# Performance work log

Hardware: AMD Instinct MI355X
Metric: run time of the kernel (lower is better)

## Reference

```python
import jax, jax.numpy as jnp
import numpy as np


def setup_inputs() -> dict:
    key = jax.random.key(0)
    ks = jax.random.split(key, 10)
    T, B, I, H, Z = 1024, 512, 128, 256, 1
    s = 0.1  # small init scale for stable recurrence
    return {
        "inputs": jax.random.normal(ks[0], (T, B, I), dtype=jnp.float32),
        "h0": jax.random.normal(ks[1], (B, H), dtype=jnp.float32) * s,
        "c0": jax.random.normal(ks[2], (B, H), dtype=jnp.float32) * s,
        "z0": jax.random.normal(ks[3], (B, Z), dtype=jnp.float32) * s,
        "W_ih": jax.random.normal(ks[4], (4 * H, I + Z), dtype=jnp.float32) * s,
        "W_hh": jax.random.normal(ks[5], (4 * H, H), dtype=jnp.float32) * s,
        "b_ih": jax.random.normal(ks[6], (4 * H,), dtype=jnp.float32) * s,
        "b_hh": jax.random.normal(ks[7], (4 * H,), dtype=jnp.float32) * s,
        "W_fc": jax.random.normal(ks[8], (Z, H), dtype=jnp.float32) * s,
        "b_fc": jax.random.normal(ks[9], (Z,), dtype=jnp.float32) * s,
    }


def reference(inputs, h0, c0, z0, W_ih, W_hh, b_ih, b_hh, W_fc, b_fc):
    def step(carry, x_t):
        h, c, z = carry
        xz = jnp.concatenate([x_t, z], axis=1)  # [B, I+Z]
        gates = xz @ W_ih.T + b_ih + h @ W_hh.T + b_hh  # [B, 4H]
        i_g, f_g, g_g, o_g = jnp.split(gates, 4, axis=1)  # torch gate order i,f,g,o
        i_g = jax.nn.sigmoid(i_g)
        f_g = jax.nn.sigmoid(f_g)
        g_g = jnp.tanh(g_g)
        o_g = jax.nn.sigmoid(o_g)
        c = f_g * c + i_g * g_g
        h = o_g * jnp.tanh(c)
        z = jnp.tanh(h @ W_fc.T + b_fc)  # [B, Z]
        return (h, c, z), z

    (h, c, _), outputs = jax.lax.scan(step, (h0, c0, z0), inputs)
    return outputs, h, c  # outputs: [T, B, Z]
```

## Files before the change

### kernel.cpp

```cpp
#include <hip/hip_runtime.h>
#include <hip/hip_bf16.h>
#include <stdint.h>

#define TT 1024
#define BB 512
#define II 128
#define HH 256
#define NKC 12
#define GSTR 132

typedef __attribute__((ext_vector_type(8))) short bf16x8;
typedef __attribute__((ext_vector_type(4))) float f32x4;
typedef __attribute__((ext_vector_type(4))) uint32_t u32x4;
typedef unsigned long long ull;

__device__ __forceinline__ float fsig(float x)  { return 1.0f / (1.0f + __expf(-x)); }
__device__ __forceinline__ float ftanh(float x) { return 1.0f - 2.0f / (__expf(2.0f * x) + 1.0f); }
__device__ __forceinline__ uint16_t f2bf(float f) {
    return __bfloat16_as_ushort(__float2bfloat16(f));
}
__device__ __forceinline__ float bf2lo(uint32_t w) { return __uint_as_float(w << 16); }
__device__ __forceinline__ float bf2hi(uint32_t w) { return __uint_as_float(w & 0xffff0000u); }

template<int DUAL>
__global__ __launch_bounds__(512, 1) void lstm_kernel(
    const float* __restrict__ x,
    const float* __restrict__ h0, const float* __restrict__ c0,
    const float* __restrict__ z0,
    const float* __restrict__ W_ih, const float* __restrict__ W_hh,
    const float* __restrict__ b_ih, const float* __restrict__ b_hh,
    const float* __restrict__ Wfc, const float* __restrict__ bfc,
    ull* __restrict__ hbF, ull* __restrict__ hbS,
    float* __restrict__ out)
{
    __shared__ __align__(16) uint16_t a_sh[NKC * 4 * 16 * 8];
    __shared__ float g_sh[16 * GSTR];
    __shared__ float zp_sh[2][8][16];

    const int tid  = threadIdx.x;
    const int lane = tid & 63, wv = tid >> 6;
    const int bid  = blockIdx.x;
    const int mm   = bid >> 3;
    const int role = mm & 7, grp = (bid & 7) * 4 + (mm >> 3);
    const int b0   = grp * 16;
    const int arow = tid >> 5, auu = tid & 31;
    const int u_g  = role * 32 + auu;
    const int xc   = (tid & 31) * 4;
    const int grole = wv, grow = (tid >> 2) & 15, gwq = tid & 3;

    bf16x8 wreg[NKC];
    {
        int lc = wv * 16 + (lane & 15);
        int col = (lc >> 5) * 256 + role * 32 + (lc & 31);
        #pragma unroll
        for (int kc = 0; kc < NKC; ++kc) {
            int k0 = kc * 32 + (lane >> 4) * 8;
            const float* src = (k0 < II) ? &W_ih[(size_t)col * (II + 1) + k0]
                                         : &W_hh[(size_t)col * HH + (k0 - II)];
            bf16x8 wv8;
            #pragma unroll
            for (int j = 0; j < 8; ++j) wv8[j] = (short)f2bf(src[j]);
            wreg[kc] = wv8;
        }
    }

    float bia[4], wzv[4];
    #pragma unroll
    for (int g = 0; g < 4; ++g) {
        int c = g * 256 + u_g;
        bia[g] = b_ih[c] + b_hh[c];
        wzv[g] = W_ih[(size_t)c * (II + 1) + II];
    }
    float wfc8[8];
    #pragma unroll
    for (int j = 0; j < 8; ++j) wfc8[j] = Wfc[grole * 32 + gwq * 8 + j];
    const float wfc  = Wfc[u_g];
    const float bfcs = bfc[0];
    const float z0r  = z0[b0 + arow];
    float c_r = c0[(size_t)(b0 + arow) * HH + u_g];

    {
        const float* hp = h0 + (size_t)(b0 + grow) * HH + grole * 32 + gwq * 8;
        uint4 pw;
        pw.x = (uint32_t)f2bf(hp[0]) | ((uint32_t)f2bf(hp[1]) << 16);
        pw.y = (uint32_t)f2bf(hp[2]) | ((uint32_t)f2bf(hp[3]) << 16);
        pw.z = (uint32_t)f2bf(hp[4]) | ((uint32_t)f2bf(hp[5]) << 16);
        pw.w = (uint32_t)f2bf(hp[6]) | ((uint32_t)f2bf(hp[7]) << 16);
        *(uint4*)&a_sh[(((4 + grole) * 4 + gwq) * 16 + grow) * 8] = pw;
    }
    {
        float4 xv = *(const float4*)&x[(size_t)(b0 + arow) * II + xc];
        int kcx = xc >> 5, gx = (xc >> 3) & 3, jx = xc & 7;
        ushort4 p;
        p.x = f2bf(xv.x); p.y = f2bf(xv.y); p.z = f2bf(xv.z); p.w = f2bf(xv.w);
        *(ushort4*)&a_sh[((kcx * 4 + gx) * 16 + arow) * 8 + jx] = p;
    }

    for (int t = 0; t <= TT; ++t) {
        float4 xn = make_float4(0.f, 0.f, 0.f, 0.f);
        if (t + 1 < TT)
            xn = *(const float4*)&x[(size_t)(t + 1) * (BB * II) + (size_t)(b0 + arow) * II + xc];

        if (t > 0 && grole != role) {
            const int par = (t - 1) & 1;
            const size_t gidx = ((((size_t)par * 32 + grp) * 8 + grole) * 16 + grow) * 16
                              + gwq * 4;
            const ull* pF = hbF + gidx;
            const ull* pS = hbS + gidx;
            u32x4 a0, a1;
            uint32_t it = 0;
            const uint32_t tt = (uint32_t)t;
            for (;;) {
                if (DUAL) {
                    u32x4 f0, f1;
                    asm volatile(
                        "global_load_dwordx4 %0, %2, off sc0\n\t"
                        "global_load_dwordx4 %1, %2, off offset:16 sc0\n\t"
                        "s_waitcnt vmcnt(0)"
                        : "=&v"(f0), "=&v"(f1) : "v"(pF) : "memory");
                    if (min(min(f0.y, f0.w), min(f1.y, f1.w)) >= tt) { a0 = f0; a1 = f1; break; }
                    ++it;
                    if ((it & 7) != 0) { __builtin_amdgcn_s_sleep(1); continue; }
                }
                u32x4 s0, s1;
                asm volatile(
                    "global_load_dwordx4 %0, %2, off sc0 sc1\n\t"
                    "global_load_dwordx4 %1, %2, off offset:16 sc0 sc1\n\t"
                    "s_waitcnt vmcnt(0)"
                    : "=&v"(s0), "=&v"(s1) : "v"(pS) : "memory");
                if (min(min(s0.y, s0.w), min(s1.y, s1.w)) >= tt) { a0 = s0; a1 = s1; break; }
                __builtin_amdgcn_s_sleep(1);
                if (!DUAL) ++it;
                if (it > (1u << 20)) { a0 = s0; a1 = s1; break; }
            }
            uint32_t w0 = a0.x, w1 = a0.z, w2 = a1.x, w3 = a1.z;
            uint4 pw; pw.x = w0; pw.y = w1; pw.z = w2; pw.w = w3;
            *(uint4*)&a_sh[(((4 + grole) * 4 + gwq) * 16 + grow) * 8] = pw;
            float p = bf2lo(w0) * wfc8[0] + bf2hi(w0) * wfc8[1]
                    + bf2lo(w1) * wfc8[2] + bf2hi(w1) * wfc8[3]
                    + bf2lo(w2) * wfc8[4] + bf2hi(w2) * wfc8[5]
                    + bf2lo(w3) * wfc8[6] + bf2hi(w3) * wfc8[7];
            p += __shfl_xor(p, 1, 64);
            p += __shfl_xor(p, 2, 64);
            if (gwq == 0) zp_sh[t & 1][grole][grow] = p;
        }
        __syncthreads();

        if (t == TT) {
            if (role == 0 && tid < 16) {
                float s = bfcs;
                #pragma unroll
                for (int r = 0; r < 8; ++r) s += zp_sh[TT & 1][r][tid];
                out[(size_t)(TT - 1) * BB + b0 + tid] = ftanh(s);
            }
            break;
        }

        f32x4 acc0 = {0.f, 0.f, 0.f, 0.f}, acc1 = {0.f, 0.f, 0.f, 0.f};
        #pragma unroll
        for (int kc = 0; kc < NKC; kc += 2) {
            bf16x8 a0 = *(const bf16x8*)&a_sh[((kc * 4 + (lane >> 4)) * 16 + (lane & 15)) * 8];
            acc0 = __builtin_amdgcn_mfma_f32_16x16x32_bf16(a0, wreg[kc], acc0, 0, 0, 0);
            bf16x8 a1 = *(const bf16x8*)&a_sh[(((kc + 1) * 4 + (lane >> 4)) * 16 + (lane & 15)) * 8];
            acc1 = __builtin_amdgcn_mfma_f32_16x16x32_bf16(a1, wreg[kc + 1], acc1, 0, 0, 0);
        }
        f32x4 acc = acc0 + acc1;
        {
            int r0 = (lane >> 4) * 4, cb = wv * 16 + (lane & 15);
            #pragma unroll
            for (int i = 0; i < 4; ++i) g_sh[(r0 + i) * GSTR + cb] = acc[i];
        }
        __syncthreads();

        {
            int kcx = xc >> 5, gx = (xc >> 3) & 3, jx = xc & 7;
            ushort4 p;
            p.x = f2bf(xn.x); p.y = f2bf(xn.y); p.z = f2bf(xn.z); p.w = f2bf(xn.w);
            *(ushort4*)&a_sh[((kcx * 4 + gx) * 16 + arow) * 8 + jx] = p;
        }

        float zp_;
        if (t == 0) {
            zp_ = z0r;
        } else {
            float s = bfcs;
            #pragma unroll
            for (int r = 0; r < 8; ++r) s += zp_sh[t & 1][r][arow];
            zp_ = ftanh(s);
            if (role == 0 && auu == 0)
                out[(size_t)(t - 1) * BB + b0 + arow] = zp_;
        }
        float gi = g_sh[arow * GSTR +      auu] + bia[0] + wzv[0] * zp_;
        float gf = g_sh[arow * GSTR + 32 + auu] + bia[1] + wzv[1] * zp_;
        float gg = g_sh[arow * GSTR + 64 + auu] + bia[2] + wzv[2] * zp_;
        float go = g_sh[arow * GSTR + 96 + auu] + bia[3] + wzv[3] * zp_;
        float ig = fsig(gi), fg = fsig(gf), gc = ftanh(gg), og = fsig(go);
        float cn = fg * c_r + ig * gc;
        c_r = cn;
        float hn = og * ftanh(cn);

        uint32_t hb16 = f2bf(hn);
        uint32_t nb = __shfl_down(hb16, 1, 64);
        if (!(auu & 1)) {
            uint32_t word = hb16 | (nb << 16);
            *(uint32_t*)&a_sh[(((4 + role) * 4 + (auu >> 3)) * 16 + arow) * 8 + (auu & 7)]
                = word;
            ull q = ((ull)(uint32_t)(t + 1) << 32) | (ull)word;
            size_t o = ((((size_t)(t & 1) * 32 + grp) * 8 + role) * 16 + arow) * 16
                     + (auu >> 1);
            if (DUAL)
                asm volatile("global_store_dwordx2 %0, %1, off sc0"
                             :: "v"(hbF + o), "v"(q) : "memory");
            asm volatile("global_store_dwordx2 %0, %1, off sc0 sc1"
                         :: "v"(hbS + o), "v"(q) : "memory");
        }
        float pz = hn * wfc;
        #pragma unroll
        for (int off = 16; off >= 1; off >>= 1) pz += __shfl_xor(pz, off, 32);
        if (auu == 0) zp_sh[(t + 1) & 1][role][arow] = pz;

        if (t == TT - 1) {
            size_t ho = (size_t)TT * BB + (size_t)(b0 + arow) * HH + u_g;
            out[ho] = hn;
            out[ho + (size_t)BB * HH] = cn;
        }
    }
}

extern "C" void kernel_launch(void* const* d_in, const int* in_sizes, int n_in,
                              void* d_out, int out_size, void* d_ws, size_t ws_size,
                              hipStream_t stream) {
    const float* x    = (const float*)d_in[0];
    const float* h0   = (const float*)d_in[1];
    const float* c0   = (const float*)d_in[2];
    const float* z0   = (const float*)d_in[3];
    const float* W_ih = (const float*)d_in[4];
    const float* W_hh = (const float*)d_in[5];
    const float* b_ih = (const float*)d_in[6];
    const float* b_hh = (const float*)d_in[7];
    const float* Wfc  = (const float*)d_in[8];
    const float* bfc  = (const float*)d_in[9];
    float* out = (float*)d_out;

    const size_t COPY = (size_t)2 * 32 * 8 * 16 * 16 * 8;
    if (ws_size >= 2 * COPY) {
        ull* hbF = (ull*)d_ws;
        ull* hbS = (ull*)((char*)d_ws + COPY);
        hipMemsetAsync(d_ws, 0, 2 * COPY, stream);
        lstm_kernel<1><<<256, 512, 0, stream>>>(x, h0, c0, z0, W_ih, W_hh,
                                                b_ih, b_hh, Wfc, bfc,
                                                hbF, hbS, out);
    } else {
        ull* hbS = (ull*)d_ws;
        hipMemsetAsync(d_ws, 0, COPY, stream);
        lstm_kernel<0><<<256, 512, 0, stream>>>(x, h0, c0, z0, W_ih, W_hh,
                                                b_ih, b_hh, Wfc, bfc,
                                                hbS, hbS, out);
    }
}
```

Before: 2.185 ms.

## Remove a barrier per step, restage x loads, and cap spin-wait fallback

Moves the x conversion and LDS store to the top of the next step, with loads issued early by only four waves, so the second __syncthreads between the MFMA and the x write is gone. The h exchange lane mapping changes so each wave's z partial reduces with cross-half shuffles, and the fast-path poll now checks the slow coherent copy every fourth iteration instead of every eighth. An adaptive cap ('strikes') shortens the spin timeout once timeouts recur, which may let a block proceed with stale data. The DUAL template is dropped, so the single-buffer fallback still issues both stores to the same buffer.

Result: slower. 2.512 ms (+14.9%).

```diff
diff --git a/kernel.cpp b/kernel.cpp
--- a/kernel.cpp
+++ b/kernel.cpp
@@ -22,7 +22,6 @@
 __device__ __forceinline__ float bf2lo(uint32_t w) { return __uint_as_float(w << 16); }
 __device__ __forceinline__ float bf2hi(uint32_t w) { return __uint_as_float(w & 0xffff0000u); }
 
-template<int DUAL>
 __global__ __launch_bounds__(512, 1) void lstm_kernel(
     const float* __restrict__ x,
     const float* __restrict__ h0, const float* __restrict__ c0,
@@ -45,8 +44,8 @@
     const int b0   = grp * 16;
     const int arow = tid >> 5, auu = tid & 31;
     const int u_g  = role * 32 + auu;
-    const int xc   = (tid & 31) * 4;
-    const int grole = wv, grow = (tid >> 2) & 15, gwq = tid & 3;
+    const int grole = wv, grow = lane & 15, gwq = lane >> 4;
+    const int xrow = lane & 15, xoct = lane >> 4;
 
     bf16x8 wreg[NKC];
     {
@@ -88,18 +87,33 @@
         pw.w = (uint32_t)f2bf(hp[6]) | ((uint32_t)f2bf(hp[7]) << 16);
         *(uint4*)&a_sh[(((4 + grole) * 4 + gwq) * 16 + grow) * 8] = pw;
     }
-    {
-        float4 xv = *(const float4*)&x[(size_t)(b0 + arow) * II + xc];
-        int kcx = xc >> 5, gx = (xc >> 3) & 3, jx = xc & 7;
-        ushort4 p;
-        p.x = f2bf(xv.x); p.y = f2bf(xv.y); p.z = f2bf(xv.z); p.w = f2bf(xv.w);
-        *(ushort4*)&a_sh[((kcx * 4 + gx) * 16 + arow) * 8 + jx] = p;
-    }
-
+    float4 xA = make_float4(0.f, 0.f, 0.f, 0.f), xB = xA;
+    if (wv < 4) {
+        const float* xs = &x[(size_t)(b0 + xrow) * II + wv * 32 + xoct * 8];
+        float4 u0 = *(const float4*)xs, u1 = *(const float4*)(xs + 4);
+        ushort4 lo, hi;
+        lo.x = f2bf(u0.x); lo.y = f2bf(u0.y); lo.z = f2bf(u0.z); lo.w = f2bf(u0.w);
+        hi.x = f2bf(u1.x); hi.y = f2bf(u1.y); hi.z = f2bf(u1.z); hi.w = f2bf(u1.w);
+        int de = ((wv * 4 + xoct) * 16 + xrow) * 8;
+        *(ushort4*)&a_sh[de] = lo;
+        *(ushort4*)&a_sh[de + 4] = hi;
+        if (TT > 1) {
+            const float* xs1 = &x[(size_t)(BB * II) + (size_t)(b0 + xrow) * II + wv * 32 + xoct * 8];
+            xA = *(const float4*)xs1;
+            xB = *(const float4*)(xs1 + 4);
+        }
+    }
+
+    uint32_t strikes = 0;
     for (int t = 0; t <= TT; ++t) {
-        float4 xn = make_float4(0.f, 0.f, 0.f, 0.f);
-        if (t + 1 < TT)
-            xn = *(const float4*)&x[(size_t)(t + 1) * (BB * II) + (size_t)(b0 + arow) * II + xc];
+        if (wv < 4 && t > 0 && t < TT) {
+            ushort4 lo, hi;
+            lo.x = f2bf(xA.x); lo.y = f2bf(xA.y); lo.z = f2bf(xA.z); lo.w = f2bf(xA.w);
+            hi.x = f2bf(xB.x); hi.y = f2bf(xB.y); hi.z = f2bf(xB.z); hi.w = f2bf(xB.w);
+            int de = ((wv * 4 + xoct) * 16 + xrow) * 8;
+            *(ushort4*)&a_sh[de] = lo;
+            *(ushort4*)&a_sh[de + 4] = hi;
+        }
 
         if (t > 0 && grole != role) {
             const int par = (t - 1) & 1;
@@ -109,19 +123,18 @@
             const ull* pS = hbS + gidx;
             u32x4 a0, a1;
             uint32_t it = 0;
+            const uint32_t cap = (strikes >= 4) ? 64u : (1u << 18);
             const uint32_t tt = (uint32_t)t;
             for (;;) {
-                if (DUAL) {
-                    u32x4 f0, f1;
-                    asm volatile(
-                        "global_load_dwordx4 %0, %2, off sc0\n\t"
-                        "global_load_dwordx4 %1, %2, off offset:16 sc0\n\t"
-                        "s_waitcnt vmcnt(0)"
-                        : "=&v"(f0), "=&v"(f1) : "v"(pF) : "memory");
-                    if (min(min(f0.y, f0.w), min(f1.y, f1.w)) >= tt) { a0 = f0; a1 = f1; break; }
-                    ++it;
-                    if ((it & 7) != 0) { __builtin_amdgcn_s_sleep(1); continue; }
-                }
+                u32x4 f0, f1;
+                asm volatile(
+                    "global_load_dwordx4 %0, %2, off sc0\n\t"
+                    "global_load_dwordx4 %1, %2, off offset:16 sc0\n\t"
+                    "s_waitcnt vmcnt(0)"
+                    : "=&v"(f0), "=&v"(f1) : "v"(pF) : "memory");
+                if (min(min(f0.y, f0.w), min(f1.y, f1.w)) >= tt) { a0 = f0; a1 = f1; break; }
+                ++it;
+                if ((it & 3) != 0) { __builtin_amdgcn_s_sleep(1); continue; }
                 u32x4 s0, s1;
                 asm volatile(
                     "global_load_dwordx4 %0, %2, off sc0 sc1\n\t"
@@ -130,8 +143,7 @@
                     : "=&v"(s0), "=&v"(s1) : "v"(pS) : "memory");
                 if (min(min(s0.y, s0.w), min(s1.y, s1.w)) >= tt) { a0 = s0; a1 = s1; break; }
                 __builtin_amdgcn_s_sleep(1);
-                if (!DUAL) ++it;
-                if (it > (1u << 20)) { a0 = s0; a1 = s1; break; }
+                if (it > cap) { ++strikes; a0 = s0; a1 = s1; break; }
             }
             uint32_t w0 = a0.x, w1 = a0.z, w2 = a1.x, w3 = a1.z;
             uint4 pw; pw.x = w0; pw.y = w1; pw.z = w2; pw.w = w3;
@@ -140,9 +152,16 @@
                     + bf2lo(w1) * wfc8[2] + bf2hi(w1) * wfc8[3]
                     + bf2lo(w2) * wfc8[4] + bf2hi(w2) * wfc8[5]
                     + bf2lo(w3) * wfc8[6] + bf2hi(w3) * wfc8[7];
-            p += __shfl_xor(p, 1, 64);
-            p += __shfl_xor(p, 2, 64);
+            p += __shfl_xor(p, 16, 64);
+            p += __shfl_xor(p, 32, 64);
             if (gwq == 0) zp_sh[t & 1][grole][grow] = p;
+        }
+
+        if (wv < 4 && t + 1 < TT) {
+            const float* xs1 = &x[(size_t)(t + 1) * (BB * II)
+                                  + (size_t)(b0 + xrow) * II + wv * 32 + xoct * 8];
+            xA = *(const float4*)xs1;
+            xB = *(const float4*)(xs1 + 4);
         }
         __syncthreads();
 
@@ -154,29 +173,6 @@
                 out[(size_t)(TT - 1) * BB + b0 + tid] = ftanh(s);
             }
             break;
-        }
-
-        f32x4 acc0 = {0.f, 0.f, 0.f, 0.f}, acc1 = {0.f, 0.f, 0.f, 0.f};
-        #pragma unroll
-        for (int kc = 0; kc < NKC; kc += 2) {
-            bf16x8 a0 = *(const bf16x8*)&a_sh[((kc * 4 + (lane >> 4)) * 16 + (lane & 15)) * 8];
-            acc0 = __builtin_amdgcn_mfma_f32_16x16x32_bf16(a0, wreg[kc], acc0, 0, 0, 0);
-            bf16x8 a1 = *(const bf16x8*)&a_sh[(((kc + 1) * 4 + (lane >> 4)) * 16 + (lane & 15)) * 8];
-            acc1 = __builtin_amdgcn_mfma_f32_16x16x32_bf16(a1, wreg[kc + 1], acc1, 0, 0, 0);
-        }
-        f32x4 acc = acc0 + acc1;
-        {
-            int r0 = (lane >> 4) * 4, cb = wv * 16 + (lane & 15);
-            #pragma unroll
-            for (int i = 0; i < 4; ++i) g_sh[(r0 + i) * GSTR + cb] = acc[i];
-        }
-        __syncthreads();
-
-        {
-            int kcx = xc >> 5, gx = (xc >> 3) & 3, jx = xc & 7;
-            ushort4 p;
-            p.x = f2bf(xn.x); p.y = f2bf(xn.y); p.z = f2bf(xn.z); p.w = f2bf(xn.w);
-            *(ushort4*)&a_sh[((kcx * 4 + gx) * 16 + arow) * 8 + jx] = p;
         }
 
         float zp_;
@@ -190,6 +186,23 @@
             if (role == 0 && auu == 0)
                 out[(size_t)(t - 1) * BB + b0 + arow] = zp_;
         }
+
+        f32x4 acc0 = {0.f, 0.f, 0.f, 0.f}, acc1 = {0.f, 0.f, 0.f, 0.f};
+        #pragma unroll
+        for (int kc = 0; kc < NKC; kc += 2) {
+            bf16x8 a0 = *(const bf16x8*)&a_sh[((kc * 4 + (lane >> 4)) * 16 + (lane & 15)) * 8];
+            acc0 = __builtin_amdgcn_mfma_f32_16x16x32_bf16(a0, wreg[kc], acc0, 0, 0, 0);
+            bf16x8 a1 = *(const bf16x8*)&a_sh[(((kc + 1) * 4 + (lane >> 4)) * 16 + (lane & 15)) * 8];
+            acc1 = __builtin_amdgcn_mfma_f32_16x16x32_bf16(a1, wreg[kc + 1], acc1, 0, 0, 0);
+        }
+        f32x4 acc = acc0 + acc1;
+        {
+            int r0 = (lane >> 4) * 4, cb = wv * 16 + (lane & 15);
+            #pragma unroll
+            for (int i = 0; i < 4; ++i) g_sh[(r0 + i) * GSTR + cb] = acc[i];
+        }
+        __syncthreads();
+
         float gi = g_sh[arow * GSTR +      auu] + bia[0] + wzv[0] * zp_;
         float gf = g_sh[arow * GSTR + 32 + auu] + bia[1] + wzv[1] * zp_;
         float gg = g_sh[arow * GSTR + 64 + auu] + bia[2] + wzv[2] * zp_;
@@ -208,9 +221,8 @@
             ull q = ((ull)(uint32_t)(t + 1) << 32) | (ull)word;
             size_t o = ((((size_t)(t & 1) * 32 + grp) * 8 + role) * 16 + arow) * 16
                      + (auu >> 1);
-            if (DUAL)
-                asm volatile("global_store_dwordx2 %0, %1, off sc0"
-                             :: "v"(hbF + o), "v"(q) : "memory");
+            asm volatile("global_store_dwordx2 %0, %1, off sc0"
+                         :: "v"(hbF + o), "v"(q) : "memory");
             asm volatile("global_store_dwordx2 %0, %1, off sc0 sc1"
                          :: "v"(hbS + o), "v"(q) : "memory");
         }
@@ -247,14 +259,12 @@
         ull* hbF = (ull*)d_ws;
         ull* hbS = (ull*)((char*)d_ws + COPY);
         hipMemsetAsync(d_ws, 0, 2 * COPY, stream);
-        lstm_kernel<1><<<256, 512, 0, stream>>>(x, h0, c0, z0, W_ih, W_hh,
-                                                b_ih, b_hh, Wfc, bfc,
-                                                hbF, hbS, out);
+        lstm_kernel<<<256, 512, 0, stream>>>(x, h0, c0, z0, W_ih, W_hh, b_ih, b_hh,
+                                             Wfc, bfc, hbF, hbS, out);
     } else {
-        ull* hbS = (ull*)d_ws;
+        ull* hb = (ull*)d_ws;
         hipMemsetAsync(d_ws, 0, COPY, stream);
-        lstm_kernel<0><<<256, 512, 0, stream>>>(x, h0, c0, z0, W_ih, W_hh,
-                                                b_ih, b_hh, Wfc, bfc,
-                                                hbS, hbS, out);
+        lstm_kernel<<<256, 512, 0, stream>>>(x, h0, c0, z0, W_ih, W_hh, b_ih, b_hh,
+                                             Wfc, bfc, hb, hb, out);
     }
 }
```

## Rework inter-block spin-wait polling, lane mapping, and single-buffer zp reduction

Applied to the files above, without the earlier changes.

Drops the DUAL template and always polls the fast (sc0) flag buffer, falling back to the system-coherent copy every fourth iteration instead of every eighth. It adds a strike counter that caps spinning at a small iteration count once timeouts have occurred. The gather lane mapping changes so the z partial reduction uses xor-16/32 shuffles, and the zp shared buffer drops double-buffering. The intent is lower cross-block handoff latency per step. The risk is that the timeout cap could consume stale h data, and the single-buffered zp_sh may race across steps.

Result: no change. 2.211 ms (+1.2%).

```diff
diff --git a/kernel.cpp b/kernel.cpp
--- a/kernel.cpp
+++ b/kernel.cpp
@@ -22,7 +22,6 @@
 __device__ __forceinline__ float bf2lo(uint32_t w) { return __uint_as_float(w << 16); }
 __device__ __forceinline__ float bf2hi(uint32_t w) { return __uint_as_float(w & 0xffff0000u); }
 
-template<int DUAL>
 __global__ __launch_bounds__(512, 1) void lstm_kernel(
     const float* __restrict__ x,
     const float* __restrict__ h0, const float* __restrict__ c0,
@@ -30,12 +29,12 @@
     const float* __restrict__ W_ih, const float* __restrict__ W_hh,
     const float* __restrict__ b_ih, const float* __restrict__ b_hh,
     const float* __restrict__ Wfc, const float* __restrict__ bfc,
-    ull* __restrict__ hbF, ull* __restrict__ hbS,
+    uint32_t* __restrict__ hbF, uint32_t* __restrict__ hbS,
     float* __restrict__ out)
 {
     __shared__ __align__(16) uint16_t a_sh[NKC * 4 * 16 * 8];
     __shared__ float g_sh[16 * GSTR];
-    __shared__ float zp_sh[2][8][16];
+    __shared__ float zp_sh[8 * 16];
 
     const int tid  = threadIdx.x;
     const int lane = tid & 63, wv = tid >> 6;
@@ -46,7 +45,7 @@
     const int arow = tid >> 5, auu = tid & 31;
     const int u_g  = role * 32 + auu;
     const int xc   = (tid & 31) * 4;
-    const int grole = wv, grow = (tid >> 2) & 15, gwq = tid & 3;
+    const int grole = wv, grow = lane & 15, gwq = lane >> 4;
 
     bf16x8 wreg[NKC];
     {
@@ -96,6 +95,7 @@
         *(ushort4*)&a_sh[((kcx * 4 + gx) * 16 + arow) * 8 + jx] = p;
     }
 
+    uint32_t strikes = 0;
     for (int t = 0; t <= TT; ++t) {
         float4 xn = make_float4(0.f, 0.f, 0.f, 0.f);
         if (t + 1 < TT)
@@ -105,23 +105,22 @@
             const int par = (t - 1) & 1;
             const size_t gidx = ((((size_t)par * 32 + grp) * 8 + grole) * 16 + grow) * 16
                               + gwq * 4;
-            const ull* pF = hbF + gidx;
-            const ull* pS = hbS + gidx;
+            const ull* pF = (const ull*)hbF + gidx;
+            const ull* pS = (const ull*)hbS + gidx;
             u32x4 a0, a1;
             uint32_t it = 0;
+            const uint32_t cap = (strikes >= 4) ? 64u : (1u << 20);
             const uint32_t tt = (uint32_t)t;
             for (;;) {
-                if (DUAL) {
-                    u32x4 f0, f1;
-                    asm volatile(
-                        "global_load_dwordx4 %0, %2, off sc0\n\t"
-                        "global_load_dwordx4 %1, %2, off offset:16 sc0\n\t"
-                        "s_waitcnt vmcnt(0)"
-                        : "=&v"(f0), "=&v"(f1) : "v"(pF) : "memory");
-                    if (min(min(f0.y, f0.w), min(f1.y, f1.w)) >= tt) { a0 = f0; a1 = f1; break; }
-                    ++it;
-                    if ((it & 7) != 0) { __builtin_amdgcn_s_sleep(1); continue; }
-                }
+                u32x4 f0, f1;
+                asm volatile(
+                    "global_load_dwordx4 %0, %2, off sc0\n\t"
+                    "global_load_dwordx4 %1, %2, off offset:16 sc0\n\t"
+                    "s_waitcnt vmcnt(0)"
+                    : "=&v"(f0), "=&v"(f1) : "v"(pF) : "memory");
+                if (min(min(f0.y, f0.w), min(f1.y, f1.w)) >= tt) { a0 = f0; a1 = f1; break; }
+                ++it;
+                if ((it & 3) != 0) { __builtin_amdgcn_s_sleep(1); continue; }
                 u32x4 s0, s1;
                 asm volatile(
                     "global_load_dwordx4 %0, %2, off sc0 sc1\n\t"
@@ -130,8 +129,7 @@
                     : "=&v"(s0), "=&v"(s1) : "v"(pS) : "memory");
                 if (min(min(s0.y, s0.w), min(s1.y, s1.w)) >= tt) { a0 = s0; a1 = s1; break; }
                 __builtin_amdgcn_s_sleep(1);
-                if (!DUAL) ++it;
-                if (it > (1u << 20)) { a0 = s0; a1 = s1; break; }
+                if (it > cap) { ++strikes; a0 = s0; a1 = s1; break; }
             }
             uint32_t w0 = a0.x, w1 = a0.z, w2 = a1.x, w3 = a1.z;
             uint4 pw; pw.x = w0; pw.y = w1; pw.z = w2; pw.w = w3;
@@ -140,9 +138,9 @@
                     + bf2lo(w1) * wfc8[2] + bf2hi(w1) * wfc8[3]
                     + bf2lo(w2) * wfc8[4] + bf2hi(w2) * wfc8[5]
                     + bf2lo(w3) * wfc8[6] + bf2hi(w3) * wfc8[7];
-            p += __shfl_xor(p, 1, 64);
-            p += __shfl_xor(p, 2, 64);
-            if (gwq == 0) zp_sh[t & 1][grole][grow] = p;
+            p += __shfl_xor(p, 16, 64);
+            p += __shfl_xor(p, 32, 64);
+            if (gwq == 0) zp_sh[grole * 16 + grow] = p;
         }
         __syncthreads();
 
@@ -150,7 +148,7 @@
             if (role == 0 && tid < 16) {
                 float s = bfcs;
                 #pragma unroll
-                for (int r = 0; r < 8; ++r) s += zp_sh[TT & 1][r][tid];
+                for (int r = 0; r < 8; ++r) s += zp_sh[r * 16 + tid];
                 out[(size_t)(TT - 1) * BB + b0 + tid] = ftanh(s);
             }
             break;
@@ -185,7 +183,7 @@
         } else {
             float s = bfcs;
             #pragma unroll
-            for (int r = 0; r < 8; ++r) s += zp_sh[t & 1][r][arow];
+            for (int r = 0; r < 8; ++r) s += zp_sh[r * 16 + arow];
             zp_ = ftanh(s);
             if (role == 0 && auu == 0)
                 out[(size_t)(t - 1) * BB + b0 + arow] = zp_;
@@ -208,16 +206,15 @@
             ull q = ((ull)(uint32_t)(t + 1) << 32) | (ull)word;
             size_t o = ((((size_t)(t & 1) * 32 + grp) * 8 + role) * 16 + arow) * 16
                      + (auu >> 1);
-            if (DUAL)
-                asm volatile("global_store_dwordx2 %0, %1, off sc0"
-                             :: "v"(hbF + o), "v"(q) : "memory");
+            asm volatile("global_store_dwordx2 %0, %1, off sc0"
+                         :: "v"((ull*)hbF + o), "v"(q) : "memory");
             asm volatile("global_store_dwordx2 %0, %1, off sc0 sc1"
-                         :: "v"(hbS + o), "v"(q) : "memory");
+                         :: "v"((ull*)hbS + o), "v"(q) : "memory");
         }
         float pz = hn * wfc;
         #pragma unroll
         for (int off = 16; off >= 1; off >>= 1) pz += __shfl_xor(pz, off, 32);
-        if (auu == 0) zp_sh[(t + 1) & 1][role][arow] = pz;
+        if (auu == 0) zp_sh[role * 16 + arow] = pz;
 
         if (t == TT - 1) {
             size_t ho = (size_t)TT * BB + (size_t)(b0 + arow) * HH + u_g;
@@ -244,17 +241,15 @@
 
     const size_t COPY = (size_t)2 * 32 * 8 * 16 * 16 * 8;
     if (ws_size >= 2 * COPY) {
-        ull* hbF = (ull*)d_ws;
-        ull* hbS = (ull*)((char*)d_ws + COPY);
+        uint32_t* hbF = (uint32_t*)d_ws;
+        uint32_t* hbS = (uint32_t*)((char*)d_ws + COPY);
         hipMemsetAsync(d_ws, 0, 2 * COPY, stream);
-        lstm_kernel<1><<<256, 512, 0, stream>>>(x, h0, c0, z0, W_ih, W_hh,
-                                                b_ih, b_hh, Wfc, bfc,
-                                                hbF, hbS, out);
+        lstm_kernel<<<256, 512, 0, stream>>>(x, h0, c0, z0, W_ih, W_hh, b_ih, b_hh,
+                                             Wfc, bfc, hbF, hbS, out);
     } else {
-        ull* hbS = (ull*)d_ws;
+        uint32_t* hb = (uint32_t*)d_ws;
         hipMemsetAsync(d_ws, 0, COPY, stream);
-        lstm_kernel<0><<<256, 512, 0, stream>>>(x, h0, c0, z0, W_ih, W_hh,
-                                                b_ih, b_hh, Wfc, bfc,
-                                                hbS, hbS, out);
+        lstm_kernel<<<256, 512, 0, stream>>>(x, h0, c0, z0, W_ih, W_hh, b_ih, b_hh,
+                                             Wfc, bfc, hb, hb, out);
     }
 }
```
